# Kernel optimization log

Hardware: AMD Instinct MI355X
Metric: run time of the kernel (lower is better)

The kernel has to match this reference:

```python
import jax, jax.numpy as jnp
import numpy as np


def setup_inputs() -> dict:
    key = jax.random.key(0)
    k1, k2, k3 = jax.random.split(key, 3)
    B, L, D = 8, 4096, 320
    CB_DIM, N_BOOKS = 16, 8192
    input_values = jax.random.normal(k1, (B, L, D), dtype=jnp.float32)
    # mask all ones -> static masked-select shape N = B*L
    mask_time_indices = jnp.ones((B, L), dtype=jnp.int32)
    # xavier_uniform for Linear(D -> CB_DIM, bias=False): limit = sqrt(6/(fan_in+fan_out))
    limit = float(np.sqrt(6.0 / (D + CB_DIM)))
    proj_weight = jax.random.uniform(k2, (CB_DIM, D), dtype=jnp.float32, minval=-limit, maxval=limit)
    code_book = jax.random.normal(k3, (N_BOOKS, CB_DIM), dtype=jnp.float32)
    return {"input_values": input_values, "mask_time_indices": mask_time_indices,
            "proj_weight": proj_weight, "code_book": code_book}


def reference(input_values, mask_time_indices, proj_weight, code_book):
    # input_values: [B, L, D]; mask is all-ones so masked select == flatten (static shape N=B*L)
    B, L, D = input_values.shape
    flat = input_values.reshape(B * L, D)  # [N, D]
    targets = flat @ proj_weight.T  # [N, cb_dim]  (random projection, no bias)
    # argmin over Euclidean norm == argmin over squared distance (monotone),
    # expanded form avoids the [N, n_books, cb_dim] broadcast intermediate.
    t2 = jnp.sum(targets * targets, axis=-1, keepdims=True)        # [N, 1]
    c2 = jnp.sum(code_book * code_book, axis=-1)                   # [n_books]
    d2 = t2 - 2.0 * (targets @ code_book.T) + c2                   # [N, n_books]
    labels = jnp.argmin(d2, axis=-1)                               # [N]
    return labels
```

## Files before the change

### kernel.cpp

```cpp
#include <hip/hip_runtime.h>

#define N_ROWS 32768
#define D_IN 320
#define CB 16
#define N_BOOKS 8192

typedef __attribute__((ext_vector_type(8))) short bf16x8;
typedef __attribute__((ext_vector_type(4))) float f32x4;
#define MFMA __builtin_amdgcn_mfma_f32_16x16x32_bf16
#define AS1 __attribute__((address_space(1)))
#define AS3 __attribute__((address_space(3)))

__device__ __forceinline__ unsigned short bf16rn(float f) {
  unsigned u = __float_as_uint(f);
  u += 0x7fffu + ((u >> 16) & 1u);
  return (unsigned short)(u >> 16);
}
__device__ __forceinline__ float bf16tof(unsigned short h) {
  return __uint_as_float(((unsigned)h) << 16);
}
__device__ __forceinline__ void gload_lds16(const short* g, short* l) {
  __builtin_amdgcn_global_load_lds((const AS1 unsigned int*)g, (AS3 unsigned int*)l, 16, 0, 0);
}

__global__ __launch_bounds__(256) void prep_kernel(const float* __restrict__ cbk,
                                                   short* __restrict__ bfrag,
                                                   float* __restrict__ nh_g,
                                                   int* __restrict__ ctr) {
  if (blockIdx.x == 0 && threadIdx.x == 0) *ctr = 0;
  const int j = blockIdx.x * 256 + threadIdx.x;
  const float4* src = (const float4*)(cbk + (size_t)j * CB);
  float4 a = src[0], b = src[1], c = src[2], d = src[3];
  float ce[16] = {a.x, a.y, a.z, a.w, b.x, b.y, b.z, b.w,
                  c.x, c.y, c.z, c.w, d.x, d.y, d.z, d.w};
  short c1[16], c2[16];
  double s = 0.0;
#pragma unroll
  for (int i = 0; i < 16; i++) {
    s += (double)ce[i] * (double)ce[i];
    unsigned short x1 = bf16rn(ce[i]);
    float r1 = ce[i] - bf16tof(x1);
    unsigned short x2 = bf16rn(r1);
    c1[i] = (short)x1; c2[i] = (short)x2;
  }
  nh_g[j] = (float)(-0.5 * s);
  bf16x8 lo1, hi1, lo2, hi2;
#pragma unroll
  for (int i = 0; i < 8; i++) {
    lo1[i] = c1[i]; hi1[i] = c1[i + 8];
    lo2[i] = c2[i]; hi2[i] = c2[i + 8];
  }
  const int bt = j >> 4, n = j & 15;
  short* base = bfrag + (size_t)bt * 1024;
  *(bf16x8*)(base + (0 * 16 + n) * 8) = lo1;
  *(bf16x8*)(base + (1 * 16 + n) * 8) = hi1;
  *(bf16x8*)(base + (2 * 16 + n) * 8) = lo1;
  *(bf16x8*)(base + (3 * 16 + n) * 8) = hi1;
  *(bf16x8*)(base + 512 + (0 * 16 + n) * 8) = lo2;
  *(bf16x8*)(base + 512 + (1 * 16 + n) * 8) = hi2;
  *(bf16x8*)(base + 512 + (2 * 16 + n) * 8) = lo2;
  *(bf16x8*)(base + 512 + (3 * 16 + n) * 8) = hi2;
}

__global__ __launch_bounds__(256, 2) void proj_kernel(const float* __restrict__ x,
                                                      const float* __restrict__ w,
                                                      short* __restrict__ tsplit) {
  __shared__ __align__(16) short wfrag[3][10][64][8];
  __shared__ __align__(16) float xs[2][64 * 36];
  const int tid = threadIdx.x;
  const int lane = tid & 63;
  const int wv = tid >> 6;

  for (int i = tid; i < D_IN * CB; i += 256) {
    int d = i >> 4, o = i & 15;
    float f = w[o * D_IN + d];
    unsigned short h1 = bf16rn(f);
    float r1 = f - bf16tof(h1);
    unsigned short h2 = bf16rn(r1);
    float r2 = r1 - bf16tof(h2);
    unsigned short h3 = bf16rn(r2);
    int c = d >> 5, qq = (d >> 3) & 3, pos = d & 7;
    int ln = qq * 16 + o;
    wfrag[0][c][ln][pos] = (short)h1;
    wfrag[1][c][ln][pos] = (short)h2;
    wfrag[2][c][ln][pos] = (short)h3;
  }

  const float* xblk = x + (size_t)blockIdx.x * 64 * D_IN;
  {
    int row = tid >> 2, k0 = (tid & 3) * 8;
    float4 v0 = *(const float4*)(xblk + row * D_IN + k0);
    float4 v1 = *(const float4*)(xblk + row * D_IN + k0 + 4);
    *(float4*)&xs[0][row * 36 + k0] = v0;
    *(float4*)&xs[0][row * 36 + k0 + 4] = v1;
  }
  __syncthreads();

  const int m = lane & 15, q = lane >> 4;
  double dacc[4] = {0.0, 0.0, 0.0, 0.0};
  for (int c = 0; c < 10; c++) {
    const int buf = c & 1;
    if (c < 9) {
      int row = tid >> 2, k0 = (tid & 3) * 8;
      float4 v0 = *(const float4*)(xblk + row * D_IN + (c + 1) * 32 + k0);
      float4 v1 = *(const float4*)(xblk + row * D_IN + (c + 1) * 32 + k0 + 4);
      *(float4*)&xs[buf ^ 1][row * 36 + k0] = v0;
      *(float4*)&xs[buf ^ 1][row * 36 + k0 + 4] = v1;
    }
    const float* xp = &xs[buf][(wv * 16 + m) * 36 + q * 8];
    float4 xa = *(const float4*)xp;
    float4 xb = *(const float4*)(xp + 4);
    float xe[8] = {xa.x, xa.y, xa.z, xa.w, xb.x, xb.y, xb.z, xb.w};
    bf16x8 a1, a2, a3;
#pragma unroll
    for (int j = 0; j < 8; j++) {
      unsigned short h1 = bf16rn(xe[j]);
      float r1 = xe[j] - bf16tof(h1);
      unsigned short h2 = bf16rn(r1);
      float r2 = r1 - bf16tof(h2);
      unsigned short h3 = bf16rn(r2);
      a1[j] = (short)h1; a2[j] = (short)h2; a3[j] = (short)h3;
    }
    bf16x8 b1 = *(const bf16x8*)wfrag[0][c][lane];
    bf16x8 b2 = *(const bf16x8*)wfrag[1][c][lane];
    bf16x8 b3 = *(const bf16x8*)wfrag[2][c][lane];
    f32x4 g = {0.f, 0.f, 0.f, 0.f};
    g = MFMA(a1, b1, g, 0, 0, 0);
#pragma unroll
    for (int r = 0; r < 4; r++) dacc[r] += (double)g[r];
    g = (f32x4){0.f, 0.f, 0.f, 0.f};
    g = MFMA(a2, b1, g, 0, 0, 0);
    g = MFMA(a1, b2, g, 0, 0, 0);
#pragma unroll
    for (int r = 0; r < 4; r++) dacc[r] += (double)g[r];
    g = (f32x4){0.f, 0.f, 0.f, 0.f};
    g = MFMA(a3, b1, g, 0, 0, 0);
    g = MFMA(a1, b3, g, 0, 0, 0);
    g = MFMA(a2, b2, g, 0, 0, 0);
#pragma unroll
    for (int r = 0; r < 4; r++) dacc[r] += (double)g[r];
    __syncthreads();
  }

  float* tl = (float*)xs;
#pragma unroll
  for (int r = 0; r < 4; r++) tl[(wv * 16 + q * 4 + r) * 17 + m] = (float)dacc[r];
  __syncthreads();
  {
    int row_l = tid >> 2, p = tid & 3;
    short h1[4], h2[4], h3[4];
#pragma unroll
    for (int i = 0; i < 4; i++) {
      float f = tl[row_l * 17 + p * 4 + i];
      unsigned short a = bf16rn(f);
      float r1 = f - bf16tof(a);
      unsigned short b = bf16rn(r1);
      float r2 = r1 - bf16tof(b);
      unsigned short cc = bf16rn(r2);
      h1[i] = (short)a; h2[i] = (short)b; h3[i] = (short)cc;
    }
    size_t base = (size_t)(blockIdx.x * 64 + row_l) * 48;
    *(short4*)(tsplit + base + p * 4) = make_short4(h1[0], h1[1], h1[2], h1[3]);
    *(short4*)(tsplit + base + 16 + p * 4) = make_short4(h2[0], h2[1], h2[2], h2[3]);
    *(short4*)(tsplit + base + 32 + p * 4) = make_short4(h3[0], h3[1], h3[2], h3[3]);
  }
}

#define SC_H 8

__global__ __launch_bounds__(256, 2) void score_kernel(const short* __restrict__ tsplit,
                                                       const short* __restrict__ bfrag,
                                                       const float* __restrict__ nh_g,
                                                       float4* __restrict__ cand) {
  __shared__ __align__(16) short ldsb[2][8192];
  __shared__ float ldsnh[1024];
  const int tid = threadIdx.x;
  const int lane = tid & 63;
  const int wv = tid >> 6;
  const int m = lane & 15, q = lane >> 4;
  const int rb = blockIdx.x & 127;
  const int h = blockIdx.x >> 7;
  const int rowbase = rb * 256;

  bf16x8 A12[4];
#pragma unroll
  for (int rt = 0; rt < 4; rt++) {
    int row = rowbase + wv * 64 + rt * 16 + m;
    A12[rt] = *(const bf16x8*)(tsplit + (size_t)row * 48 + q * 8);
  }
  for (int i = tid; i < 1024; i += 256) ldsnh[i] = nh_g[h * 1024 + i];

  const short* gq = bfrag + (size_t)h * 65536;
  {
    const short* g0 = gq + wv * 512 + lane * 8;
#pragma unroll
    for (int it = 0; it < 4; it++)
      gload_lds16(g0 + it * 2048, &ldsb[0][it * 2048 + wv * 512]);
  }

  float s1[4][4], s2[4][4];
  int i1[4][4];
#pragma unroll
  for (int rt = 0; rt < 4; rt++)
#pragma unroll
    for (int r = 0; r < 4; r++) { s1[rt][r] = -3.4e38f; s2[rt][r] = -3.4e38f; i1[rt][r] = 0; }

  __syncthreads();

  for (int sc = 0; sc < 8; sc++) {
    const int cur = sc & 1;
    if (sc < 7) {
      const short* gs = gq + (sc + 1) * 8192 + wv * 512 + lane * 8;
#pragma unroll
      for (int it = 0; it < 4; it++)
        gload_lds16(gs + it * 2048, &ldsb[cur ^ 1][it * 2048 + wv * 512]);
    }
#pragma unroll
    for (int bt = 0; bt < 8; bt++) {
      const short* bp = &ldsb[cur][bt * 1024];
      bf16x8 b1 = *(const bf16x8*)(bp + lane * 8);
      bf16x8 b2 = *(const bf16x8*)(bp + 512 + lane * 8);
      const int btg = sc * 8 + bt;
      float nh0 = ldsnh[btg * 16 + m];
      f32x4 ci = {nh0, nh0, nh0, nh0};
      const int colv = h * 1024 + btg * 16 + m;
#pragma unroll
      for (int rt = 0; rt < 4; rt++) {
        f32x4 acc = MFMA(A12[rt], b1, ci, 0, 0, 0);
        acc = MFMA(A12[rt], b2, acc, 0, 0, 0);
#pragma unroll
        for (int r = 0; r < 4; r++) {
          float v = acc[r];
          float s1o = s1[rt][r];
          s2[rt][r] = __builtin_amdgcn_fmed3f(v, s1o, s2[rt][r]);
          s1[rt][r] = fmaxf(s1o, v);
          i1[rt][r] = (v > s1o) ? colv : i1[rt][r];
        }
      }
    }
    __syncthreads();
  }

#pragma unroll
  for (int rt = 0; rt < 4; rt++)
#pragma unroll
    for (int r = 0; r < 4; r++) {
      float a1v = s1[rt][r], a2v = s2[rt][r];
      int ai = i1[rt][r];
#pragma unroll
      for (int msk = 1; msk <= 8; msk <<= 1) {
        float o1 = __shfl_xor(a1v, msk);
        float o2 = __shfl_xor(a2v, msk);
        int oi = __shfl_xor(ai, msk);
        if (o1 > a1v) {
          a2v = fmaxf(a1v, o2); a1v = o1; ai = oi;
        } else {
          a2v = fmaxf(a2v, o1);
          if (o1 == a1v && oi < ai) ai = oi;
        }
      }
      if (m == 0) {
        int row = rowbase + wv * 64 + rt * 16 + q * 4 + r;
        cand[(size_t)h * N_ROWS + row] = make_float4(a1v, a2v, __int_as_float(ai), 0.f);
      }
    }
}

#define MARGIN_EPS 1.0e-3f

__global__ __launch_bounds__(256) void merge_flag_kernel(const float4* __restrict__ cand,
                                                         int* __restrict__ out,
                                                         int* __restrict__ list,
                                                         int* __restrict__ ctr) {
  const int r = blockIdx.x * 256 + threadIdx.x;
  float S1 = -3.4e38f, S2 = -3.4e38f;
  int I = 0;
#pragma unroll
  for (int h = 0; h < SC_H; h++) {
    float4 v = cand[(size_t)h * N_ROWS + r];
    if (v.x > S1) {
      S2 = fmaxf(S1, v.y); S1 = v.x; I = __float_as_int(v.z);
    } else {
      S2 = fmaxf(S2, v.x);
    }
  }
  out[r] = I;
  if (S1 - S2 < MARGIN_EPS) {
    int slot = atomicAdd(ctr, 1);
    list[slot] = r;
  }
}

__global__ __launch_bounds__(256) void rescore_kernel(const int* __restrict__ list,
                                                      const int* __restrict__ ctr,
                                                      const float* __restrict__ x,
                                                      const float* __restrict__ w,
                                                      const float* __restrict__ codebook,
                                                      int* __restrict__ out) {
  __shared__ double ps[16][17];
  __shared__ double tsh[16];
  __shared__ double rs[256];
  __shared__ int ri[256];
  const int tid = threadIdx.x;
  const int total = ctr[0];

  for (int it = blockIdx.x; it < total; it += gridDim.x) {
    const int row = list[it];
    {
      int o = tid & 15, c = tid >> 4;
      double p = 0.0;
      for (int k = 0; k < 20; k++) {
        int d = c * 20 + k;
        p = fma((double)x[(size_t)row * D_IN + d], (double)w[o * D_IN + d], p);
      }
      ps[c][o] = p;
    }
    __syncthreads();
    if (tid < 16) {
      double t = 0.0;
      for (int c = 0; c < 16; c++) t += ps[c][tid];
      tsh[tid] = t;
    }
    __syncthreads();
    double t[16];
#pragma unroll
    for (int i = 0; i < 16; i++) t[i] = tsh[i];
    double bs = -1.0e300;
    int bi = 0;
    for (int j = tid; j < N_BOOKS; j += 256) {
      const float* cp = codebook + (size_t)j * CB;
      double dot = 0.0, cc = 0.0;
#pragma unroll
      for (int i = 0; i < 16; i++) {
        double cv = (double)cp[i];
        dot = fma(t[i], cv, dot);
        cc = fma(cv, cv, cc);
      }
      double mv = dot - 0.5 * cc;
      if (mv > bs) { bs = mv; bi = j; }
    }
    rs[tid] = bs; ri[tid] = bi;
    __syncthreads();
    for (int s = 128; s > 0; s >>= 1) {
      if (tid < s) {
        double os = rs[tid + s]; int oi = ri[tid + s];
        if (os > rs[tid] || (os == rs[tid] && oi < ri[tid])) { rs[tid] = os; ri[tid] = oi; }
      }
      __syncthreads();
    }
    if (tid == 0) out[row] = ri[0];
    __syncthreads();
  }
}

extern "C" void kernel_launch(void* const* d_in, const int* in_sizes, int n_in,
                              void* d_out, int out_size, void* d_ws, size_t ws_size,
                              hipStream_t stream) {
  (void)in_sizes; (void)n_in; (void)out_size; (void)ws_size;
  const float* x = (const float*)d_in[0];
  const float* w = (const float*)d_in[2];
  const float* codebook = (const float*)d_in[3];

  char* ws = (char*)d_ws;
  short* tsplit = (short*)(ws);
  short* bfrag = (short*)(ws + (3 << 20));
  float* nh_g = (float*)(ws + (4 << 20));
  int* list = (int*)(ws + 4231168);
  int* ctr = (int*)(ws + 4362240);
  float4* cand = (float4*)(ws + (5 << 20));
  int* out = (int*)d_out;

  prep_kernel<<<N_BOOKS / 256, 256, 0, stream>>>(codebook, bfrag, nh_g, ctr);
  proj_kernel<<<N_ROWS / 64, 256, 0, stream>>>(x, w, tsplit);
  score_kernel<<<128 * SC_H, 256, 0, stream>>>(tsplit, bfrag, nh_g, cand);
  merge_flag_kernel<<<N_ROWS / 256, 256, 0, stream>>>(cand, out, list, ctr);
  rescore_kernel<<<512, 256, 0, stream>>>(list, ctr, x, w, codebook, out);
}
```

Baseline: 182.3 us.

## Fuse codebook prep into projection kernel and split score kernel into more column slices

```diff
diff --git a/kernel.cpp b/kernel.cpp
--- a/kernel.cpp
+++ b/kernel.cpp
@@ -23,51 +23,52 @@
   __builtin_amdgcn_global_load_lds((const AS1 unsigned int*)g, (AS3 unsigned int*)l, 16, 0, 0);
 }
 
-__global__ __launch_bounds__(256) void prep_kernel(const float* __restrict__ cbk,
-                                                   short* __restrict__ bfrag,
-                                                   float* __restrict__ nh_g,
-                                                   int* __restrict__ ctr) {
-  if (blockIdx.x == 0 && threadIdx.x == 0) *ctr = 0;
-  const int j = blockIdx.x * 256 + threadIdx.x;
-  const float4* src = (const float4*)(cbk + (size_t)j * CB);
-  float4 a = src[0], b = src[1], c = src[2], d = src[3];
-  float ce[16] = {a.x, a.y, a.z, a.w, b.x, b.y, b.z, b.w,
-                  c.x, c.y, c.z, c.w, d.x, d.y, d.z, d.w};
-  short c1[16], c2[16];
-  double s = 0.0;
-#pragma unroll
-  for (int i = 0; i < 16; i++) {
-    s += (double)ce[i] * (double)ce[i];
-    unsigned short x1 = bf16rn(ce[i]);
-    float r1 = ce[i] - bf16tof(x1);
-    unsigned short x2 = bf16rn(r1);
-    c1[i] = (short)x1; c2[i] = (short)x2;
-  }
-  nh_g[j] = (float)(-0.5 * s);
-  bf16x8 lo1, hi1, lo2, hi2;
-#pragma unroll
-  for (int i = 0; i < 8; i++) {
-    lo1[i] = c1[i]; hi1[i] = c1[i + 8];
-    lo2[i] = c2[i]; hi2[i] = c2[i + 8];
-  }
-  const int bt = j >> 4, n = j & 15;
-  short* base = bfrag + (size_t)bt * 1024;
-  *(bf16x8*)(base + (0 * 16 + n) * 8) = lo1;
-  *(bf16x8*)(base + (1 * 16 + n) * 8) = hi1;
-  *(bf16x8*)(base + (2 * 16 + n) * 8) = lo1;
-  *(bf16x8*)(base + (3 * 16 + n) * 8) = hi1;
-  *(bf16x8*)(base + 512 + (0 * 16 + n) * 8) = lo2;
-  *(bf16x8*)(base + 512 + (1 * 16 + n) * 8) = hi2;
-  *(bf16x8*)(base + 512 + (2 * 16 + n) * 8) = lo2;
-  *(bf16x8*)(base + 512 + (3 * 16 + n) * 8) = hi2;
-}
-
-__global__ __launch_bounds__(256, 2) void proj_kernel(const float* __restrict__ x,
-                                                      const float* __restrict__ w,
-                                                      short* __restrict__ tsplit) {
+__global__ __launch_bounds__(256, 2) void proj_prep_kernel(
+    const float* __restrict__ x, const float* __restrict__ w, short* __restrict__ tsplit,
+    const float* __restrict__ cbk, short* __restrict__ bfrag, float* __restrict__ nh_g,
+    int* __restrict__ ctr) {
   __shared__ __align__(16) short wfrag[3][10][64][8];
   __shared__ __align__(16) float xs[2][64 * 36];
   const int tid = threadIdx.x;
+
+  if (blockIdx.x >= 512) {
+    const int bid = blockIdx.x - 512;
+    if (bid == 0 && tid == 0) *ctr = 0;
+    const int j = bid * 256 + tid;
+    const float4* src = (const float4*)(cbk + (size_t)j * CB);
+    float4 a = src[0], b = src[1], c = src[2], d = src[3];
+    float ce[16] = {a.x, a.y, a.z, a.w, b.x, b.y, b.z, b.w,
+                    c.x, c.y, c.z, c.w, d.x, d.y, d.z, d.w};
+    short c1[16], c2[16];
+    double s = 0.0;
+#pragma unroll
+    for (int i = 0; i < 16; i++) {
+      s += (double)ce[i] * (double)ce[i];
+      unsigned short x1 = bf16rn(ce[i]);
+      float r1 = ce[i] - bf16tof(x1);
+      unsigned short x2 = bf16rn(r1);
+      c1[i] = (short)x1; c2[i] = (short)x2;
+    }
+    nh_g[j] = (float)(-0.5 * s);
+    bf16x8 lo1, hi1, lo2, hi2;
+#pragma unroll
+    for (int i = 0; i < 8; i++) {
+      lo1[i] = c1[i]; hi1[i] = c1[i + 8];
+      lo2[i] = c2[i]; hi2[i] = c2[i + 8];
+    }
+    const int bt = j >> 4, n = j & 15;
+    short* base = bfrag + (size_t)bt * 1024;
+    *(bf16x8*)(base + (0 * 16 + n) * 8) = lo1;
+    *(bf16x8*)(base + (1 * 16 + n) * 8) = hi1;
+    *(bf16x8*)(base + (2 * 16 + n) * 8) = lo1;
+    *(bf16x8*)(base + (3 * 16 + n) * 8) = hi1;
+    *(bf16x8*)(base + 512 + (0 * 16 + n) * 8) = lo2;
+    *(bf16x8*)(base + 512 + (1 * 16 + n) * 8) = hi2;
+    *(bf16x8*)(base + 512 + (2 * 16 + n) * 8) = lo2;
+    *(bf16x8*)(base + 512 + (3 * 16 + n) * 8) = hi2;
+    return;
+  }
+
   const int lane = tid & 63;
   const int wv = tid >> 6;
 
@@ -97,7 +98,7 @@
   __syncthreads();
 
   const int m = lane & 15, q = lane >> 4;
-  double dacc[4] = {0.0, 0.0, 0.0, 0.0};
+  f32x4 g1 = {0.f, 0.f, 0.f, 0.f}, g2 = {0.f, 0.f, 0.f, 0.f}, g3 = {0.f, 0.f, 0.f, 0.f};
   for (int c = 0; c < 10; c++) {
     const int buf = c & 1;
     if (c < 9) {
@@ -124,27 +125,21 @@
     bf16x8 b1 = *(const bf16x8*)wfrag[0][c][lane];
     bf16x8 b2 = *(const bf16x8*)wfrag[1][c][lane];
     bf16x8 b3 = *(const bf16x8*)wfrag[2][c][lane];
-    f32x4 g = {0.f, 0.f, 0.f, 0.f};
-    g = MFMA(a1, b1, g, 0, 0, 0);
-#pragma unroll
-    for (int r = 0; r < 4; r++) dacc[r] += (double)g[r];
-    g = (f32x4){0.f, 0.f, 0.f, 0.f};
-    g = MFMA(a2, b1, g, 0, 0, 0);
-    g = MFMA(a1, b2, g, 0, 0, 0);
-#pragma unroll
-    for (int r = 0; r < 4; r++) dacc[r] += (double)g[r];
-    g = (f32x4){0.f, 0.f, 0.f, 0.f};
-    g = MFMA(a3, b1, g, 0, 0, 0);
-    g = MFMA(a1, b3, g, 0, 0, 0);
-    g = MFMA(a2, b2, g, 0, 0, 0);
-#pragma unroll
-    for (int r = 0; r < 4; r++) dacc[r] += (double)g[r];
+    g1 = MFMA(a1, b1, g1, 0, 0, 0);
+    g2 = MFMA(a2, b1, g2, 0, 0, 0);
+    g2 = MFMA(a1, b2, g2, 0, 0, 0);
+    g3 = MFMA(a3, b1, g3, 0, 0, 0);
+    g3 = MFMA(a1, b3, g3, 0, 0, 0);
+    g3 = MFMA(a2, b2, g3, 0, 0, 0);
     __syncthreads();
   }
 
   float* tl = (float*)xs;
 #pragma unroll
-  for (int r = 0; r < 4; r++) tl[(wv * 16 + q * 4 + r) * 17 + m] = (float)dacc[r];
+  for (int r = 0; r < 4; r++) {
+    double t = (double)g1[r] + ((double)g2[r] + (double)g3[r]);
+    tl[(wv * 16 + q * 4 + r) * 17 + m] = (float)t;
+  }
   __syncthreads();
   {
     int row_l = tid >> 2, p = tid & 3;
@@ -166,14 +161,14 @@
   }
 }
 
-#define SC_H 8
-
-__global__ __launch_bounds__(256, 2) void score_kernel(const short* __restrict__ tsplit,
+#define SC_H 16
+
+__global__ __launch_bounds__(256, 4) void score_kernel(const short* __restrict__ tsplit,
                                                        const short* __restrict__ bfrag,
                                                        const float* __restrict__ nh_g,
                                                        float4* __restrict__ cand) {
-  __shared__ __align__(16) short ldsb[2][8192];
-  __shared__ float ldsnh[1024];
+  __shared__ __align__(16) short ldsb[2][4096];
+  __shared__ float ldsnh[512];
   const int tid = threadIdx.x;
   const int lane = tid & 63;
   const int wv = tid >> 6;
@@ -188,13 +183,13 @@
     int row = rowbase + wv * 64 + rt * 16 + m;
     A12[rt] = *(const bf16x8*)(tsplit + (size_t)row * 48 + q * 8);
   }
-  for (int i = tid; i < 1024; i += 256) ldsnh[i] = nh_g[h * 1024 + i];
-
-  const short* gq = bfrag + (size_t)h * 65536;
+  for (int i = tid; i < 512; i += 256) ldsnh[i] = nh_g[h * 512 + i];
+
+  const short* gq = bfrag + (size_t)h * 32768;
   {
     const short* g0 = gq + wv * 512 + lane * 8;
 #pragma unroll
-    for (int it = 0; it < 4; it++)
+    for (int it = 0; it < 2; it++)
       gload_lds16(g0 + it * 2048, &ldsb[0][it * 2048 + wv * 512]);
   }
 
@@ -210,20 +205,20 @@
   for (int sc = 0; sc < 8; sc++) {
     const int cur = sc & 1;
     if (sc < 7) {
-      const short* gs = gq + (sc + 1) * 8192 + wv * 512 + lane * 8;
-#pragma unroll
-      for (int it = 0; it < 4; it++)
+      const short* gs = gq + (sc + 1) * 4096 + wv * 512 + lane * 8;
+#pragma unroll
+      for (int it = 0; it < 2; it++)
         gload_lds16(gs + it * 2048, &ldsb[cur ^ 1][it * 2048 + wv * 512]);
     }
 #pragma unroll
-    for (int bt = 0; bt < 8; bt++) {
+    for (int bt = 0; bt < 4; bt++) {
       const short* bp = &ldsb[cur][bt * 1024];
       bf16x8 b1 = *(const bf16x8*)(bp + lane * 8);
       bf16x8 b2 = *(const bf16x8*)(bp + 512 + lane * 8);
-      const int btg = sc * 8 + bt;
+      const int btg = sc * 4 + bt;
       float nh0 = ldsnh[btg * 16 + m];
       f32x4 ci = {nh0, nh0, nh0, nh0};
-      const int colv = h * 1024 + btg * 16 + m;
+      const int colv = h * 512 + btg * 16 + m;
 #pragma unroll
       for (int rt = 0; rt < 4; rt++) {
         f32x4 acc = MFMA(A12[rt], b1, ci, 0, 0, 0);
@@ -370,8 +365,8 @@
   float4* cand = (float4*)(ws + (5 << 20));
   int* out = (int*)d_out;
 
-  prep_kernel<<<N_BOOKS / 256, 256, 0, stream>>>(codebook, bfrag, nh_g, ctr);
-  proj_kernel<<<N_ROWS / 64, 256, 0, stream>>>(x, w, tsplit);
+  proj_prep_kernel<<<512 + N_BOOKS / 256, 256, 0, stream>>>(x, w, tsplit, codebook, bfrag,
+                                                            nh_g, ctr);
   score_kernel<<<128 * SC_H, 256, 0, stream>>>(tsplit, bfrag, nh_g, cand);
   merge_flag_kernel<<<N_ROWS / 256, 256, 0, stream>>>(cand, out, list, ctr);
   rescore_kernel<<<512, 256, 0, stream>>>(list, ctr, x, w, codebook, out);
```

New measurement: 190.2 us. +4.3%, slower.
